# Optimization experiments

Hardware: AMD Instinct MI355X
Metric: run time of the kernel (lower is better)

The kernel has to match this reference:

```python
import jax, jax.numpy as jnp
import numpy as np

NF = 16            # num_frequencies
S = 2              # scale_factor
MAX_STD = 0.5
POS_LIMIT = 1.0


def setup_inputs() -> dict:
    key = jax.random.key(0)
    ks = jax.random.split(key, 8)
    B, G, H, W = 16, 256, 128, 128
    hidden, base = 1024, 256
    in_dim = (G + 2 * NF + 1) * S * S  # 4624
    # xavier-uniform-like scales
    lim1 = float(np.sqrt(6.0 / (hidden + in_dim)))
    lim2 = float(np.sqrt(6.0 / (base + hidden)))
    return {
        "position": jax.random.uniform(ks[0], (B, 4), dtype=jnp.float32),
        "gestalt": jax.random.normal(ks[1], (B, G), dtype=jnp.float32),
        "mask": jax.random.uniform(ks[2], (B, 1, H, W), dtype=jnp.float32),
        "depth": jax.random.normal(ks[3], (B, 1, H, W), dtype=jnp.float32),
        "weight1": jax.random.uniform(ks[4], (hidden, in_dim), minval=-lim1, maxval=lim1, dtype=jnp.float32),
        "bias1": jnp.zeros((hidden,), dtype=jnp.float32),
        "weight2": jax.random.uniform(ks[5], (base, hidden), minval=-lim2, maxval=lim2, dtype=jnp.float32),
        "bias2": jnp.zeros((base,), dtype=jnp.float32),
    }


def reference(position, gestalt, mask, depth, weight1, bias1, weight2, bias2):
    B, _, H, W = mask.shape
    # positional grids in [-1, 1], shapes (1,1,H,W)
    gx = (jnp.arange(W, dtype=jnp.float32) / (W - 1)) * 2 - 1
    gy = (jnp.arange(H, dtype=jnp.float32) / (H - 1)) * 2 - 1
    grid_y, grid_x = jnp.meshgrid(gy, gx, indexing="ij")
    grid_x = grid_x[None, None]
    grid_y = grid_y[None, None]

    x = jnp.clip(position[:, 0], -POS_LIMIT, POS_LIMIT)[:, None, None, None]
    y = jnp.clip(position[:, 1], -POS_LIMIT, POS_LIMIT)[:, None, None, None]
    min_std = 1.0 / min(H, W)
    std = 0.1 / jnp.clip(position[:, 3], min_std, MAX_STD)[:, None, None, None]
    std_y = std
    std_x = std * (W / H)

    half_pi = jnp.float32(np.pi / 2)
    ngx = (grid_x - x) * std_x * half_pi  # (B,1,H,W)
    ngy = (grid_y - y) * std_y * half_pi
    freqs = (2.0 ** jnp.arange(NF, dtype=jnp.float32))[None, :, None, None]
    cos_x = jnp.cos(ngx * freqs)  # (B,NF,H,W)
    cos_y = jnp.cos(ngy * freqs)
    # interleave: [cx0, cy0, cx1, cy1, ...]
    embedding = jnp.stack([cos_x, cos_y], axis=2).reshape(B, 2 * NF, H, W)

    inp = jnp.concatenate(
        [gestalt[:, :, None, None] * mask, embedding * mask, depth * mask], axis=1
    )  # (B,C,H,W)
    C = inp.shape[1]
    # space-to-depth patchify
    p = inp.reshape(B, C, H // S, S, W // S, S)
    p = p.transpose(0, 2, 4, 1, 3, 5).reshape(B * (H // S) * (W // S), C * S * S)

    h = p @ weight1.T + bias1
    h = h * jax.nn.sigmoid(h)  # SiLU
    o = h @ weight2.T + bias2
    return o.reshape(B, H // S, W // S, -1).transpose(0, 3, 1, 2)
```

## Files before the change

### kernel.cpp

```cpp
#include <hip/hip_runtime.h>
#include <cstdio>


#define NFREQ 16
#define BB 16
#define G 256
#define KIN 1156
#define K1 144
#define STAGE_U16 12800
#define NSTAGE 3

typedef unsigned short u16;
using bf16x8 = __bf16 __attribute__((ext_vector_type(8)));
using f32x16 = float __attribute__((ext_vector_type(16)));
using f32x4  = float __attribute__((ext_vector_type(4)));

__device__ __forceinline__ u16 f2bf(float f) {
  unsigned u = __float_as_uint(f);
  u += 0x7fffu + ((u >> 16) & 1u);
  return (u16)(u >> 16);
}
__device__ __forceinline__ unsigned pk2(float a, float b) {
  return (unsigned)f2bf(a) | ((unsigned)f2bf(b) << 16);
}
__device__ __forceinline__ unsigned pk2f(float a, float b) {
  unsigned ua = __float_as_uint(a) + 0x8000u;
  unsigned ub = __float_as_uint(b) + 0x8000u;
  return __builtin_amdgcn_perm(ub, ua, 0x07060302u);
}
__device__ __forceinline__ float silu(float h) {
  float e = __builtin_amdgcn_exp2f(h * -1.44269504088896f);
  return h * __builtin_amdgcn_rcpf(1.f + e);
}
__device__ __forceinline__ void gl_lds16(const u16* g, u16* l) {
  __builtin_amdgcn_global_load_lds(
      (const __attribute__((address_space(1))) void*)g,
      (__attribute__((address_space(3))) void*)l, 16, 0, 0);
}

__global__ void k_pre(const float* __restrict__ pos,
                      const float* __restrict__ gestalt,
                      const float* __restrict__ w1,
                      const float* __restrict__ w2,
                      const float* __restrict__ bias1,
                      float* __restrict__ cosx, float* __restrict__ cosy,
                      u16* __restrict__ B1F, u16* __restrict__ W2F) {
  const int bid = blockIdx.x;
  const int t = threadIdx.x;

  if (bid < 1024) {
    __shared__ float w1row[KIN];
    __shared__ float gestT[G * 17];
    __shared__ float psum[256];
    __shared__ float wg[64];
    const int n = bid;
    const float b1v = bias1[n];
#pragma unroll
    for (int i = t; i < KIN; i += 256) w1row[i] = w1[(size_t)n * KIN + i];
#pragma unroll
    for (int i = t; i < BB * G; i += 256) {
      int bb = i >> 8, c = i & 255;
      gestT[c * 17 + bb] = gestalt[i];
    }
    __syncthreads();
    {
      int bb = t & 15, j = (t >> 4) & 3, q = t >> 6;
      float acc = 0.f;
#pragma unroll 8
      for (int c = q * 64; c < q * 64 + 64; ++c)
        acc += gestT[c * 17 + bb] * w1row[4 * c + j];
      psum[t] = acc;
    }
    __syncthreads();
    if (t < 64) {
      int bb = t >> 2, j = t & 3;
      wg[t] = psum[j * 16 + bb] + psum[64 + j * 16 + bb] +
              psum[128 + j * 16 + bb] + psum[192 + j * 16 + bb];
    }
    __syncthreads();
    const int ch = n >> 5, l31n = n & 31;
    for (int c = t; c < BB * (K1 / 8); c += 256) {
      int bb = c / 18, kc = c - bb * 18;
      int k0 = kc * 8;
      float v[8];
#pragma unroll
      for (int i = 0; i < 8; ++i) {
        int k = k0 + i;
        float vv;
        if (k < 64)       vv = w1row[1024 + 8 * (k >> 2) + (k & 3)];
        else if (k < 128) { int kk = k - 64; vv = w1row[1024 + 8 * (kk >> 2) + 4 + (kk & 3)]; }
        else if (k < 132) vv = wg[bb * 4 + (k - 128)];
        else if (k < 136) vv = w1row[1152 + (k - 132)];
        else if (k == 136) vv = b1v;
        else              vv = 0.f;
        v[i] = vv;
      }
      uint4 u;
      u.x = pk2(v[0], v[1]); u.y = pk2(v[2], v[3]);
      u.z = pk2(v[4], v[5]); u.w = pk2(v[6], v[7]);
      size_t idx0 = ((((size_t)bb * 32 + ch) * 9 + (kc >> 1)) * 64 +
                     (kc & 1) * 32 + l31n) * 8;
      *(uint4*)(B1F + idx0) = u;
    }
  } else if (bid < 1152) {
    int e8 = (bid - 1024) * 256 + t;
    int lane = e8 & 63;
    int ct   = (e8 >> 6) & 7;
    int kc   = e8 >> 9;
    int n2 = ct * 32 + (lane & 31);
    int k2 = kc * 16 + (lane >> 5) * 8;
    const float* src = w2 + (size_t)n2 * 1024 + k2;
    uint4 u;
    u.x = pk2(src[0], src[1]); u.y = pk2(src[2], src[3]);
    u.z = pk2(src[4], src[5]); u.w = pk2(src[6], src[7]);
    *(uint4*)(W2F + (size_t)e8 * 8) = u;
  } else {
    int idx = (bid - 1152) * 256 + t;
    int table = idx >> 15;
    int rem = idx & 32767;
    int b = rem >> 11;
    int f = (rem >> 7) & 15;
    int c = rem & 127;
    float p0 = pos[b * 4 + 0];
    float p1 = pos[b * 4 + 1];
    float p3 = pos[b * 4 + 3];
    float x = fminf(fmaxf(p0, -1.f), 1.f);
    float y = fminf(fmaxf(p1, -1.f), 1.f);
    float stdv = 0.1f / fminf(fmaxf(p3, 0.0078125f), 0.5f);
    const float half_pi = 1.57079632679489661923f;
    float g = ((float)c / 127.0f) * 2.0f - 1.0f;
    float ng = (table == 0) ? ((g - x) * stdv) * half_pi
                            : ((g - y) * stdv) * half_pi;
    float freq = (float)(1 << f);
    float val = cosf(ng * freq);
    if (table == 0) cosx[(b * NFREQ + f) * 128 + c] = val;
    else            cosy[(b * NFREQ + f) * 128 + c] = val;
  }
}

__global__ __launch_bounds__(256, 2) void k_main(
    const u16* __restrict__ B1F, const u16* __restrict__ W2F,
    const float* __restrict__ mask, const float* __restrict__ depth,
    const float* __restrict__ cosx, const float* __restrict__ cosy,
    const float* __restrict__ bias2, float* __restrict__ out)
{
  __shared__ __align__(16) u16 sbuf[NSTAGE * STAGE_U16];
  float* stg = (float*)sbuf;

  const int tid = threadIdx.x;
  const int w = tid >> 6;
  const int lane = tid & 63;
  const int l31 = lane & 31;
  const int lhi = lane >> 5;
  const int bswz = (blockIdx.x & 7) * 64 + (blockIdx.x >> 3);
  const int r0 = bswz * 128;
  const int b = r0 >> 12;
  const int oy0 = (r0 >> 6) & 63;

  {
    const float4* cx4 = (const float4*)(cosx + (size_t)b * 2048);
    ((float4*)stg)[tid]       = cx4[tid];
    ((float4*)stg)[tid + 256] = cx4[tid + 256];
    if (tid < 64)
      stg[2048 + tid] = cosy[((size_t)b * 16 + (tid >> 2)) * 128 + 2 * oy0 + (tid & 3)];
    if (tid < 128) {
      ((float4*)(stg + 2112))[tid] = ((const float4*)(mask  + ((size_t)b * 128 + 2 * oy0) * 128))[tid];
      ((float4*)(stg + 2624))[tid] = ((const float4*)(depth + ((size_t)b * 128 + 2 * oy0) * 128))[tid];
    }
  }
  __syncthreads();

  bf16x8 bfr[9];
  {
    const int r = w * 32 + l31;
    const int oyl = r >> 6, ox = r & 63;
    float m[4], dd[4];
#pragma unroll
    for (int j = 0; j < 4; ++j) {
      int sy = j >> 1, sx = j & 1;
      float mv = stg[2112 + (2 * oyl + sy) * 128 + 2 * ox + sx];
      m[j] = mv;
      dd[j] = stg[2624 + (2 * oyl + sy) * 128 + 2 * ox + sx] * mv;
    }
#pragma unroll
    for (int ks = 0; ks < 9; ++ks) {
      const int k0 = ks * 16 + lhi * 8;
      unsigned dwords[4];
#pragma unroll
      for (int h = 0; h < 4; ++h) {
        float v[2];
#pragma unroll
        for (int p = 0; p < 2; ++p) {
          const int k = k0 + 2 * h + p;
          float vv;
          if (k < 64) {
            const int f = k >> 2, j = k & 3;
            vv = m[j] * stg[f * 128 + 2 * ox + (j & 1)];
          } else if (k < 128) {
            const int kk = k - 64, f = kk >> 2, j = kk & 3;
            vv = m[j] * stg[2048 + f * 4 + 2 * oyl + (j >> 1)];
          } else if (k < 132) {
            vv = m[k - 128];
          } else if (k < 136) {
            vv = dd[k - 132];
          } else if (k == 136) {
            vv = 1.0f;
          } else {
            vv = 0.f;
          }
          v[p] = vv;
        }
        dwords[h] = pk2(v[0], v[1]);
      }
      uint4 u; u.x = dwords[0]; u.y = dwords[1]; u.z = dwords[2]; u.w = dwords[3];
      bfr[ks] = __builtin_bit_cast(bf16x8, u);
    }
  }
  __syncthreads();

  f32x16 acc2[8];
#pragma unroll
  for (int c = 0; c < 8; ++c)
#pragma unroll
    for (int i = 0; i < 16; ++i) acc2[c][i] = 0.f;

  const int naf = (w == 0) ? 3 : 2;
  const int wf0 = 9 + ((w + 3) & 3);
  const u16* b1base = B1F + (size_t)b * 32 * 4608 + lane * 8;
  const u16* w2base = W2F + lane * 8;

  auto prefetch = [&](int ch, u16* dst) {
    const u16* asrc = b1base + (size_t)ch * 4608;
    const u16* wsrc = w2base + (size_t)ch * 8192;
#pragma unroll
    for (int j = 0; j < 3; ++j)
      if (j < naf) gl_lds16(asrc + (w + 4 * j) * 512, dst + (w + 4 * j) * 512);
#pragma unroll
    for (int j = 0; j < 4; ++j) {
      const int c = wf0 + 4 * j;
      gl_lds16(wsrc + (c - 9) * 512, dst + c * 512);
    }
  };

  prefetch(0, sbuf);
  prefetch(1, sbuf + STAGE_U16);

  int st = 0;
  for (int ch = 0; ch < 32; ++ch) {
    if (ch < 31) asm volatile("s_waitcnt vmcnt(6)" ::: "memory");
    else         asm volatile("s_waitcnt vmcnt(0)" ::: "memory");
    __builtin_amdgcn_s_barrier();
    asm volatile("" ::: "memory");
    __builtin_amdgcn_sched_barrier(0);

    if (ch + 2 < 32) {
      int s2 = st + 2; if (s2 >= NSTAGE) s2 -= NSTAGE;
      prefetch(ch + 2, sbuf + s2 * STAGE_U16);
    }

    const u16* afb = sbuf + st * STAGE_U16;
    const u16* wfb = afb + 4608;

    f32x16 a1a, a1b;
#pragma unroll
    for (int i = 0; i < 16; ++i) { a1a[i] = 0.f; a1b[i] = 0.f; }
#pragma unroll
    for (int ks = 0; ks < 4; ++ks) {
      bf16x8 af0 = *(const bf16x8*)(afb + (2 * ks) * 512 + lane * 8);
      bf16x8 af1 = *(const bf16x8*)(afb + (2 * ks + 1) * 512 + lane * 8);
      a1a = __builtin_amdgcn_mfma_f32_32x32x16_bf16(af0, bfr[2 * ks],     a1a, 0, 0, 0);
      a1b = __builtin_amdgcn_mfma_f32_32x32x16_bf16(af1, bfr[2 * ks + 1], a1b, 0, 0, 0);
    }
    {
      bf16x8 af8 = *(const bf16x8*)(afb + 8 * 512 + lane * 8);
      a1a = __builtin_amdgcn_mfma_f32_32x32x16_bf16(af8, bfr[8], a1a, 0, 0, 0);
    }

    unsigned d[8];
#pragma unroll
    for (int q = 0; q < 4; ++q) {
      float s0 = silu(a1a[4 * q + 0] + a1b[4 * q + 0]);
      float s1 = silu(a1a[4 * q + 1] + a1b[4 * q + 1]);
      float s2 = silu(a1a[4 * q + 2] + a1b[4 * q + 2]);
      float s3 = silu(a1a[4 * q + 3] + a1b[4 * q + 3]);
      d[2 * q]     = pk2f(s0, s1);
      d[2 * q + 1] = pk2f(s2, s3);
    }
    unsigned e0 = d[0], e1 = d[2];
    unsigned e2 = d[1], e3 = d[3];
    unsigned e4 = d[4], e5 = d[6];
    unsigned e6 = d[5], e7 = d[7];
    asm("v_permlane32_swap_b32 %0, %1" : "+v"(e0), "+v"(e1));
    asm("v_permlane32_swap_b32 %0, %1" : "+v"(e2), "+v"(e3));
    asm("v_permlane32_swap_b32 %0, %1" : "+v"(e4), "+v"(e5));
    asm("v_permlane32_swap_b32 %0, %1" : "+v"(e6), "+v"(e7));
    uint4 fav, fbv;
    fav.x = e0; fav.y = e2; fav.z = e1; fav.w = e3;
    fbv.x = e4; fbv.y = e6; fbv.z = e5; fbv.w = e7;
    bf16x8 fragA = __builtin_bit_cast(bf16x8, fav);
    bf16x8 fragB = __builtin_bit_cast(bf16x8, fbv);

#pragma unroll
    for (int ct = 0; ct < 8; ++ct) {
      bf16x8 wf = *(const bf16x8*)(wfb + ct * 512 + lane * 8);
      acc2[ct] = __builtin_amdgcn_mfma_f32_32x32x16_bf16(fragA, wf, acc2[ct], 0, 0, 0);
    }
#pragma unroll
    for (int ct = 0; ct < 8; ++ct) {
      bf16x8 wf = *(const bf16x8*)(wfb + 4096 + ct * 512 + lane * 8);
      acc2[ct] = __builtin_amdgcn_mfma_f32_32x32x16_bf16(fragB, wf, acc2[ct], 0, 0, 0);
    }

    if (++st == NSTAGE) st = 0;
  }

#pragma unroll
  for (int ct = 0; ct < 8; ++ct) {
    const int n2 = ct * 32 + l31;
    const float b2 = bias2[n2];
    float* ob = out + ((size_t)b * 256 + n2) * 4096;
#pragma unroll
    for (int q = 0; q < 4; ++q) {
      const int rl = w * 32 + 8 * q + 4 * lhi;
      const int oy = oy0 + (rl >> 6);
      const int ox = rl & 63;
      f32x4 v;
      v[0] = acc2[ct][4 * q + 0] + b2;
      v[1] = acc2[ct][4 * q + 1] + b2;
      v[2] = acc2[ct][4 * q + 2] + b2;
      v[3] = acc2[ct][4 * q + 3] + b2;
      *(f32x4*)(ob + oy * 64 + ox) = v;
    }
  }
}


extern "C" void kernel_launch(void* const* d_in, const int* in_sizes, int n_in,
                              void* d_out, int out_size, void* d_ws, size_t ws_size,
                              hipStream_t stream) {
  const float* pos     = (const float*)d_in[0];
  const float* gestalt = (const float*)d_in[1];
  const float* mask    = (const float*)d_in[2];
  const float* depth   = (const float*)d_in[3];
  const float* w1      = (const float*)d_in[4];
  const float* bias1   = (const float*)d_in[5];
  const float* w2      = (const float*)d_in[6];
  const float* bias2   = (const float*)d_in[7];
  float* out = (float*)d_out;

  const size_t NEED = 131072u + 131072u + 4718592u + 524288u;
  if (ws_size < NEED) {
    fprintf(stderr, "[kernel] ws_size=%zu < needed %zu — skipping launches\n",
            ws_size, NEED);
    return;
  }
  char* ws = (char*)d_ws;
  float* cosx = (float*)(ws);
  float* cosy = (float*)(ws + 131072);
  u16*   B1F  = (u16*)(ws + 262144);
  u16*   W2F  = (u16*)(ws + 262144 + 4718592);

  k_pre<<<1408, 256, 0, stream>>>(pos, gestalt, w1, w2, bias1, cosx, cosy, B1F, W2F);
  k_main<<<512, 256, 0, stream>>>(B1F, W2F, mask, depth, cosx, cosy, bias2, out);
}
```

Baseline: 157.9 us.

## Software-pipeline GEMM1 of next chunk with GEMM2 of previous chunk

Restructures the main chunk loop so each iteration issues GEMM1 for chunk ch back to back with GEMM2 for chunk ch-1, with SiLU packing placed after the barrier and the prefetch. This breaks the serial dependency GEMM1 -> SiLU -> GEMM2 inside one iteration, giving the MFMA pipe independent work. It also raises wave priority with s_setprio around the MFMA bursts and drops the explicit accumulator zeroing in favour of a shared zero operand. In exchange the wait becomes vmcnt(0) every iteration and a stage buffer stays live one iteration longer, which could expose load latency or race if the stage indexing is wrong.

```diff
diff --git a/kernel.cpp b/kernel.cpp
--- a/kernel.cpp
+++ b/kernel.cpp
@@ -138,6 +138,69 @@
   }
 }
 
+
+__device__ __forceinline__ f32x16 mfma_bf16(bf16x8 a, bf16x8 b, f32x16 c) {
+  return __builtin_amdgcn_mfma_f32_32x32x16_bf16(a, b, c, 0, 0, 0);
+}
+
+__device__ __forceinline__ void gemm1(const u16* afb, const bf16x8* bfr, int lane8,
+                                      const f32x16& ZERO, f32x16& a1a, f32x16& a1b) {
+  bf16x8 af0 = *(const bf16x8*)(afb + 0 * 512 + lane8);
+  bf16x8 af1 = *(const bf16x8*)(afb + 1 * 512 + lane8);
+  a1a = mfma_bf16(af0, bfr[0], ZERO);
+  a1b = mfma_bf16(af1, bfr[1], ZERO);
+#pragma unroll
+  for (int ks = 1; ks < 4; ++ks) {
+    bf16x8 afa = *(const bf16x8*)(afb + (2 * ks) * 512 + lane8);
+    bf16x8 afc = *(const bf16x8*)(afb + (2 * ks + 1) * 512 + lane8);
+    a1a = mfma_bf16(afa, bfr[2 * ks], a1a);
+    a1b = mfma_bf16(afc, bfr[2 * ks + 1], a1b);
+  }
+  bf16x8 af8 = *(const bf16x8*)(afb + 8 * 512 + lane8);
+  a1a = mfma_bf16(af8, bfr[8], a1a);
+}
+
+__device__ __forceinline__ void gemm2(const u16* wfb, int lane8,
+                                      bf16x8 fA, bf16x8 fB, f32x16* acc2) {
+#pragma unroll
+  for (int ct = 0; ct < 8; ++ct) {
+    bf16x8 wf = *(const bf16x8*)(wfb + ct * 512 + lane8);
+    acc2[ct] = mfma_bf16(fA, wf, acc2[ct]);
+  }
+#pragma unroll
+  for (int ct = 0; ct < 8; ++ct) {
+    bf16x8 wf = *(const bf16x8*)(wfb + 4096 + ct * 512 + lane8);
+    acc2[ct] = mfma_bf16(fB, wf, acc2[ct]);
+  }
+}
+
+__device__ __forceinline__ void silupack(const f32x16& a1a, const f32x16& a1b,
+                                         bf16x8& fragA, bf16x8& fragB) {
+  unsigned d[8];
+#pragma unroll
+  for (int q = 0; q < 4; ++q) {
+    float s0 = silu(a1a[4 * q + 0] + a1b[4 * q + 0]);
+    float s1 = silu(a1a[4 * q + 1] + a1b[4 * q + 1]);
+    float s2 = silu(a1a[4 * q + 2] + a1b[4 * q + 2]);
+    float s3 = silu(a1a[4 * q + 3] + a1b[4 * q + 3]);
+    d[2 * q]     = pk2f(s0, s1);
+    d[2 * q + 1] = pk2f(s2, s3);
+  }
+  unsigned e0 = d[0], e1 = d[2];
+  unsigned e2 = d[1], e3 = d[3];
+  unsigned e4 = d[4], e5 = d[6];
+  unsigned e6 = d[5], e7 = d[7];
+  asm("v_permlane32_swap_b32 %0, %1" : "+v"(e0), "+v"(e1));
+  asm("v_permlane32_swap_b32 %0, %1" : "+v"(e2), "+v"(e3));
+  asm("v_permlane32_swap_b32 %0, %1" : "+v"(e4), "+v"(e5));
+  asm("v_permlane32_swap_b32 %0, %1" : "+v"(e6), "+v"(e7));
+  uint4 fav, fbv;
+  fav.x = e0; fav.y = e2; fav.z = e1; fav.w = e3;
+  fbv.x = e4; fbv.y = e6; fbv.z = e5; fbv.w = e7;
+  fragA = __builtin_bit_cast(bf16x8, fav);
+  fragB = __builtin_bit_cast(bf16x8, fbv);
+}
+
 __global__ __launch_bounds__(256, 2) void k_main(
     const u16* __restrict__ B1F, const u16* __restrict__ W2F,
     const float* __restrict__ mask, const float* __restrict__ depth,
@@ -150,6 +213,7 @@
   const int tid = threadIdx.x;
   const int w = tid >> 6;
   const int lane = tid & 63;
+  const int lane8 = lane * 8;
   const int l31 = lane & 31;
   const int lhi = lane >> 5;
   const int bswz = (blockIdx.x & 7) * 64 + (blockIdx.x >> 3);
@@ -224,95 +288,76 @@
 #pragma unroll
     for (int i = 0; i < 16; ++i) acc2[c][i] = 0.f;
 
+  f32x16 ZERO;
+#pragma unroll
+  for (int i = 0; i < 16; ++i) ZERO[i] = 0.f;
+
   const int naf = (w == 0) ? 3 : 2;
   const int wf0 = 9 + ((w + 3) & 3);
-  const u16* b1base = B1F + (size_t)b * 32 * 4608 + lane * 8;
-  const u16* w2base = W2F + lane * 8;
-
-  auto prefetch = [&](int ch, u16* dst) {
-    const u16* asrc = b1base + (size_t)ch * 4608;
-    const u16* wsrc = w2base + (size_t)ch * 8192;
+  const u16* apre = B1F + (size_t)b * 32 * 4608 + lane8;
+  const u16* wpre = W2F + lane8;
+
+  auto prefetchP = [&](u16* dst) {
 #pragma unroll
     for (int j = 0; j < 3; ++j)
-      if (j < naf) gl_lds16(asrc + (w + 4 * j) * 512, dst + (w + 4 * j) * 512);
+      if (j < naf) gl_lds16(apre + (w + 4 * j) * 512, dst + (w + 4 * j) * 512);
 #pragma unroll
     for (int j = 0; j < 4; ++j) {
       const int c = wf0 + 4 * j;
-      gl_lds16(wsrc + (c - 9) * 512, dst + c * 512);
-    }
+      gl_lds16(wpre + (c - 9) * 512, dst + c * 512);
+    }
+    apre += 4608; wpre += 8192;
   };
 
-  prefetch(0, sbuf);
-  prefetch(1, sbuf + STAGE_U16);
-
-  int st = 0;
-  for (int ch = 0; ch < 32; ++ch) {
-    if (ch < 31) asm volatile("s_waitcnt vmcnt(6)" ::: "memory");
-    else         asm volatile("s_waitcnt vmcnt(0)" ::: "memory");
+  prefetchP(sbuf);
+  prefetchP(sbuf + STAGE_U16);
+  asm volatile("s_waitcnt vmcnt(6)" ::: "memory");
+  __builtin_amdgcn_s_barrier();
+  asm volatile("" ::: "memory");
+  __builtin_amdgcn_sched_barrier(0);
+
+  bf16x8 fragA, fragB;
+
+  {
+    f32x16 a1a, a1b;
+    __builtin_amdgcn_s_setprio(1);
+    gemm1(sbuf, bfr, lane8, ZERO, a1a, a1b);
+    __builtin_amdgcn_s_setprio(0);
+    asm volatile("s_waitcnt vmcnt(0)" ::: "memory");
     __builtin_amdgcn_s_barrier();
     asm volatile("" ::: "memory");
     __builtin_amdgcn_sched_barrier(0);
+    prefetchP(sbuf + 2 * STAGE_U16);
+    silupack(a1a, a1b, fragA, fragB);
+  }
+
+  int st = 1;
+  for (int ch = 1; ch < 32; ++ch) {
+    const u16* afb  = sbuf + st * STAGE_U16;
+    const int  stp  = (st == 0) ? 2 : st - 1;
+    const u16* wfbp = sbuf + stp * STAGE_U16 + 4608;
+
+    f32x16 a1a, a1b;
+    __builtin_amdgcn_s_setprio(1);
+    gemm1(afb, bfr, lane8, ZERO, a1a, a1b);
+    gemm2(wfbp, lane8, fragA, fragB, acc2);
+    __builtin_amdgcn_s_setprio(0);
+
+    asm volatile("s_waitcnt vmcnt(0)" ::: "memory");
+    __builtin_amdgcn_s_barrier();
+    asm volatile("" ::: "memory");
+    __builtin_amdgcn_sched_barrier(0);
 
     if (ch + 2 < 32) {
       int s2 = st + 2; if (s2 >= NSTAGE) s2 -= NSTAGE;
-      prefetch(ch + 2, sbuf + s2 * STAGE_U16);
-    }
-
-    const u16* afb = sbuf + st * STAGE_U16;
-    const u16* wfb = afb + 4608;
-
-    f32x16 a1a, a1b;
-#pragma unroll
-    for (int i = 0; i < 16; ++i) { a1a[i] = 0.f; a1b[i] = 0.f; }
-#pragma unroll
-    for (int ks = 0; ks < 4; ++ks) {
-      bf16x8 af0 = *(const bf16x8*)(afb + (2 * ks) * 512 + lane * 8);
-      bf16x8 af1 = *(const bf16x8*)(afb + (2 * ks + 1) * 512 + lane * 8);
-      a1a = __builtin_amdgcn_mfma_f32_32x32x16_bf16(af0, bfr[2 * ks],     a1a, 0, 0, 0);
-      a1b = __builtin_amdgcn_mfma_f32_32x32x16_bf16(af1, bfr[2 * ks + 1], a1b, 0, 0, 0);
-    }
-    {
-      bf16x8 af8 = *(const bf16x8*)(afb + 8 * 512 + lane * 8);
-      a1a = __builtin_amdgcn_mfma_f32_32x32x16_bf16(af8, bfr[8], a1a, 0, 0, 0);
-    }
-
-    unsigned d[8];
-#pragma unroll
-    for (int q = 0; q < 4; ++q) {
-      float s0 = silu(a1a[4 * q + 0] + a1b[4 * q + 0]);
-      float s1 = silu(a1a[4 * q + 1] + a1b[4 * q + 1]);
-      float s2 = silu(a1a[4 * q + 2] + a1b[4 * q + 2]);
-      float s3 = silu(a1a[4 * q + 3] + a1b[4 * q + 3]);
-      d[2 * q]     = pk2f(s0, s1);
-      d[2 * q + 1] = pk2f(s2, s3);
-    }
-    unsigned e0 = d[0], e1 = d[2];
-    unsigned e2 = d[1], e3 = d[3];
-    unsigned e4 = d[4], e5 = d[6];
-    unsigned e6 = d[5], e7 = d[7];
-    asm("v_permlane32_swap_b32 %0, %1" : "+v"(e0), "+v"(e1));
-    asm("v_permlane32_swap_b32 %0, %1" : "+v"(e2), "+v"(e3));
-    asm("v_permlane32_swap_b32 %0, %1" : "+v"(e4), "+v"(e5));
-    asm("v_permlane32_swap_b32 %0, %1" : "+v"(e6), "+v"(e7));
-    uint4 fav, fbv;
-    fav.x = e0; fav.y = e2; fav.z = e1; fav.w = e3;
-    fbv.x = e4; fbv.y = e6; fbv.z = e5; fbv.w = e7;
-    bf16x8 fragA = __builtin_bit_cast(bf16x8, fav);
-    bf16x8 fragB = __builtin_bit_cast(bf16x8, fbv);
-
-#pragma unroll
-    for (int ct = 0; ct < 8; ++ct) {
-      bf16x8 wf = *(const bf16x8*)(wfb + ct * 512 + lane * 8);
-      acc2[ct] = __builtin_amdgcn_mfma_f32_32x32x16_bf16(fragA, wf, acc2[ct], 0, 0, 0);
-    }
-#pragma unroll
-    for (int ct = 0; ct < 8; ++ct) {
-      bf16x8 wf = *(const bf16x8*)(wfb + 4096 + ct * 512 + lane * 8);
-      acc2[ct] = __builtin_amdgcn_mfma_f32_32x32x16_bf16(fragB, wf, acc2[ct], 0, 0, 0);
-    }
-
+      prefetchP(sbuf + s2 * STAGE_U16);
+    }
+
+    silupack(a1a, a1b, fragA, fragB);
     if (++st == NSTAGE) st = 0;
   }
+
+  gemm2(sbuf + 1 * STAGE_U16 + 4608, lane8, fragA, fragB, acc2);
 
 #pragma unroll
   for (int ct = 0; ct < 8; ++ct) {
```

Result: no change. 158.4 us (+0.4%).
